# Kernel tuning notes

Hardware: AMD Instinct MI355X
Metric: run time of the kernel (lower is better)

The kernel has to match this reference:

```python
import jax, jax.numpy as jnp
import numpy as np

B, T, D, H = 2, 2048, 1024, 16
DH = D // H

def setup_inputs() -> dict:
    key = jax.random.key(0)
    ks = jax.random.split(key, 6)
    s = 0.02
    return {
        "x": jax.random.normal(ks[0], (B, T, D), jnp.float32),
        "Wq": jax.random.normal(ks[1], (D, D), jnp.float32) * s,
        "Wk": jax.random.normal(ks[2], (D, D), jnp.float32) * s,
        "Wv": jax.random.normal(ks[3], (D, D), jnp.float32) * s,
        "Wo": jax.random.normal(ks[4], (D, D), jnp.float32) * s,
        "bo": jnp.zeros((D,), jnp.float32),
    }

def reference(x, Wq, Wk, Wv, Wo, bo):
    Bx, Tx, _ = x.shape
    # project and split heads: [B, H, T, DH]
    q = (x @ Wq).reshape(Bx, Tx, H, DH).transpose(0, 2, 1, 3)
    k = (x @ Wk).reshape(Bx, Tx, H, DH).transpose(0, 2, 1, 3)
    v = (x @ Wv).reshape(Bx, Tx, H, DH).transpose(0, 2, 1, 3)
    scores = jnp.einsum("bhqd,bhkd->bhqk", q, k)  # [B,H,T,T]
    causal = jnp.triu(jnp.ones((Tx, Tx), bool), k=1)  # True above diagonal
    scores = jnp.where(causal, -jnp.inf, scores)
    # original scales AFTER masking (equivalent math)
    w = jax.nn.softmax(scores / jnp.sqrt(jnp.float32(DH)), axis=-1)
    # dropout p=0.0 -> identity
    ctx = jnp.einsum("bhqk,bhkd->bhqd", w, v)
    ctx = ctx.transpose(0, 2, 1, 3).reshape(Bx, Tx, D)
    return ctx @ Wo + bo
```

## Files before the change

kernel.cpp:

```cpp
#include <hip/hip_runtime.h>
#include <hip/hip_bf16.h>


typedef __bf16 bf16x8 __attribute__((ext_vector_type(8)));
typedef __bf16 bf16x4 __attribute__((ext_vector_type(4)));
typedef float  f32x4  __attribute__((ext_vector_type(4)));

#define Bx 2
#define Tx 2048
#define Dx 1024
#define Hx 16
#define DHx 64

__global__ __launch_bounds__(256) void prep(const float* __restrict__ x,
                                            const float* __restrict__ W0,
                                            const float* __restrict__ W1,
                                            const float* __restrict__ W2,
                                            const float* __restrict__ W3,
                                            __bf16* __restrict__ xb,
                                            __bf16* __restrict__ Wt) {
    const int z = blockIdx.z;
    if (z == 0) {
        const int blk = blockIdx.y * 16 + blockIdx.x;
        const float* xp = x + (size_t)blk * 16384;
        __bf16* xo = xb + (size_t)blk * 16384;
#pragma unroll
        for (int i = 0; i < 16; i++) {
            float4 v = *(const float4*)(xp + i * 1024 + threadIdx.x * 4);
            bf16x4 o;
            o[0] = (__bf16)v.x; o[1] = (__bf16)v.y; o[2] = (__bf16)v.z; o[3] = (__bf16)v.w;
            *(bf16x4*)(xo + i * 1024 + threadIdx.x * 4) = o;
        }
        return;
    }
    __shared__ float tile[64][65];
    const float* W = (z == 1) ? W0 : (z == 2) ? W1 : (z == 3) ? W2 : W3;
    __bf16* o = Wt + (size_t)(z - 1) * Dx * Dx;
    int k0 = blockIdx.x * 64, n0 = blockIdx.y * 64;
    int t = threadIdx.x;
    int cc = t & 63, rbase = t >> 6;
#pragma unroll
    for (int i = 0; i < 16; i++) {
        int rr = rbase + i * 4;
        tile[rr][cc] = W[(size_t)(k0 + rr) * Dx + n0 + cc];
    }
    __syncthreads();
#pragma unroll
    for (int i = 0; i < 16; i++) {
        int rr = rbase + i * 4;
        o[(size_t)(n0 + rr) * Dx + k0 + cc] = (__bf16)tile[cc][rr];
    }
}

static __device__ __forceinline__ void gload16(const __bf16* g, __bf16* l) {
    __builtin_amdgcn_global_load_lds((const __attribute__((address_space(1))) void*)g,
                                     (__attribute__((address_space(3))) void*)l, 16, 0, 0);
}

__global__ __launch_bounds__(256, 3) void gemm_qkv(const __bf16* __restrict__ A,
                                                   const __bf16* __restrict__ BT,
                                                   __bf16* __restrict__ Qb,
                                                   __bf16* __restrict__ Kb,
                                                   __bf16* __restrict__ Vt) {
    __shared__ __bf16 As[2][128 * 32];
    __shared__ __bf16 Bs[2][128 * 32];
    const int t = threadIdx.x;
    const int lane = t & 63, wave = t >> 6;
    const int lane15 = lane & 15, quad = lane >> 4;
    const int m0 = blockIdx.x * 128, n0 = blockIdx.y * 128;
    const int wm = wave & 1, wn = wave >> 1;

    const int sr = wave * 16 + (lane >> 2);
    const int sc = (lane & 3) * 8;
    const __bf16* Ag = A + (size_t)(m0 + sr) * Dx + sc;
    const __bf16* Bg = BT + (size_t)(n0 + sr) * Dx + sc;
    __bf16* As00 = &As[0][(wave * 16) * 32];
    __bf16* As01 = &As[0][(64 + wave * 16) * 32];
    __bf16* As10 = &As[1][(wave * 16) * 32];
    __bf16* As11 = &As[1][(64 + wave * 16) * 32];
    __bf16* Bs00 = &Bs[0][(wave * 16) * 32];
    __bf16* Bs01 = &Bs[0][(64 + wave * 16) * 32];
    __bf16* Bs10 = &Bs[1][(wave * 16) * 32];
    __bf16* Bs11 = &Bs[1][(64 + wave * 16) * 32];

    f32x4 acc[4][4];
#pragma unroll
    for (int i = 0; i < 4; i++)
#pragma unroll
        for (int j = 0; j < 4; j++) acc[i][j] = (f32x4){0.f, 0.f, 0.f, 0.f};

    for (int k0 = 0; k0 < Dx; k0 += 64) {
        gload16(Ag, As00);
        gload16(Ag + 64 * Dx, As01);
        gload16(Ag + 32, As10);
        gload16(Ag + 64 * Dx + 32, As11);
        gload16(Bg, Bs00);
        gload16(Bg + 64 * Dx, Bs01);
        gload16(Bg + 32, Bs10);
        gload16(Bg + 64 * Dx + 32, Bs11);
        Ag += 64; Bg += 64;
        __syncthreads();
#pragma unroll
        for (int half = 0; half < 2; half++) {
            bf16x8 af[4], bfr[4];
#pragma unroll
            for (int i = 0; i < 4; i++)
                af[i] = *(const bf16x8*)&As[half][(wm * 64 + i * 16 + lane15) * 32 + quad * 8];
#pragma unroll
            for (int j = 0; j < 4; j++)
                bfr[j] = *(const bf16x8*)&Bs[half][(wn * 64 + j * 16 + lane15) * 32 + quad * 8];
#pragma unroll
            for (int mt = 0; mt < 4; mt++)
#pragma unroll
                for (int nt = 0; nt < 4; nt++)
                    acc[mt][nt] = __builtin_amdgcn_mfma_f32_16x16x32_bf16(af[mt], bfr[nt], acc[mt][nt], 0, 0, 0);
        }
        __syncthreads();
    }

    const int z = n0 >> 10;
    if (z < 2) {
        __bf16* outp = z ? Kb : Qb;
        const float scale = z ? 1.0f : 0.18033688011112042f;
#pragma unroll
        for (int mt = 0; mt < 4; mt++)
#pragma unroll
            for (int nt = 0; nt < 4; nt++) {
                const int cc = (n0 + wn * 64 + nt * 16 + lane15) & 1023;
                const int h = cc >> 6, dh = cc & 63;
#pragma unroll
                for (int r4 = 0; r4 < 4; r4++) {
                    const int row = m0 + wm * 64 + mt * 16 + quad * 4 + r4;
                    const int b = row >> 11, tt = row & 2047;
                    outp[(((size_t)(b * Hx + h) * Tx + tt) << 6) + dh] =
                        (__bf16)(acc[mt][nt][r4] * scale);
                }
            }
    } else {
#pragma unroll
        for (int mt = 0; mt < 4; mt++)
#pragma unroll
            for (int nt = 0; nt < 4; nt++) {
                const int cc = (n0 + wn * 64 + nt * 16 + lane15) & 1023;
                const int h = cc >> 6, dh = cc & 63;
#pragma unroll
                for (int r4 = 0; r4 < 4; r4++) {
                    const int row = m0 + wm * 64 + mt * 16 + quad * 4 + r4;
                    const int b = row >> 11, tt = row & 2047;
                    Vt[((size_t)(b * Hx + h) * DHx + dh) * Tx + tt] = (__bf16)acc[mt][nt][r4];
                }
            }
    }
}

__global__ __launch_bounds__(256, 2) void gemm_out(const __bf16* __restrict__ A,
                                                   const __bf16* __restrict__ BT,
                                                   float* __restrict__ outf,
                                                   const float* __restrict__ bias) {
    __shared__ __bf16 As[2][128 * 32];
    __shared__ __bf16 Bs[2][64 * 32];
    const int t = threadIdx.x;
    const int lane = t & 63, wave = t >> 6;
    const int lane15 = lane & 15, quad = lane >> 4;
    const int m0 = blockIdx.x * 128, n0 = blockIdx.y * 64;
    const int wm = wave & 1, wn = wave >> 1;

    const int sr = wave * 16 + (lane >> 2), sc = (lane & 3) * 8;
    const __bf16* Ag = A + (size_t)(m0 + sr) * Dx + sc;
    const __bf16* Bg = BT + (size_t)(n0 + sr) * Dx + sc;
    __bf16* As00 = &As[0][(wave * 16) * 32];
    __bf16* As01 = &As[0][(64 + wave * 16) * 32];
    __bf16* As10 = &As[1][(wave * 16) * 32];
    __bf16* As11 = &As[1][(64 + wave * 16) * 32];
    __bf16* Bs0  = &Bs[0][(wave * 16) * 32];
    __bf16* Bs1  = &Bs[1][(wave * 16) * 32];

    f32x4 acc[4][2];
#pragma unroll
    for (int i = 0; i < 4; i++)
#pragma unroll
        for (int j = 0; j < 2; j++) acc[i][j] = (f32x4){0.f, 0.f, 0.f, 0.f};

    for (int k0 = 0; k0 < Dx; k0 += 64) {
        gload16(Ag, As00);
        gload16(Ag + 64 * Dx, As01);
        gload16(Ag + 32, As10);
        gload16(Ag + 64 * Dx + 32, As11);
        gload16(Bg, Bs0);
        gload16(Bg + 32, Bs1);
        Ag += 64; Bg += 64;
        __syncthreads();
#pragma unroll
        for (int half = 0; half < 2; half++) {
            bf16x8 af[4], bfr[2];
#pragma unroll
            for (int i = 0; i < 4; i++)
                af[i] = *(const bf16x8*)&As[half][(wm * 64 + i * 16 + lane15) * 32 + quad * 8];
#pragma unroll
            for (int j = 0; j < 2; j++)
                bfr[j] = *(const bf16x8*)&Bs[half][(wn * 32 + j * 16 + lane15) * 32 + quad * 8];
#pragma unroll
            for (int mt = 0; mt < 4; mt++)
#pragma unroll
                for (int nt = 0; nt < 2; nt++)
                    acc[mt][nt] = __builtin_amdgcn_mfma_f32_16x16x32_bf16(af[mt], bfr[nt], acc[mt][nt], 0, 0, 0);
        }
        __syncthreads();
    }

#pragma unroll
    for (int mt = 0; mt < 4; mt++)
#pragma unroll
        for (int nt = 0; nt < 2; nt++) {
            const int col = n0 + wn * 32 + nt * 16 + lane15;
#pragma unroll
            for (int r4 = 0; r4 < 4; r4++) {
                const int row = m0 + wm * 64 + mt * 16 + quad * 4 + r4;
                outf[(size_t)row * Dx + col] = acc[mt][nt][r4] + bias[col];
            }
        }
}

__global__ __launch_bounds__(256) void attn_mfma(const __bf16* __restrict__ Q,
                                                 const __bf16* __restrict__ K,
                                                 const __bf16* __restrict__ Vt,
                                                 __bf16* __restrict__ ctx) {
    __shared__ __bf16 Ks[2][64 * 72];
    __shared__ __bf16 Vs[2][64 * 72];
    __shared__ __bf16 Ps[64 * 72];
    const int t = threadIdx.x;
    const int lane = t & 63, wave = t >> 6;
    const int lane15 = lane & 15, quad = lane >> 4;
    const int id = blockIdx.x;
    const int bh = id & 31, p = id >> 5;
    const int b = bh >> 4, h = bh & 15;
    const size_t headoff = ((size_t)(b * Hx + h)) * Tx * DHx;
    const __bf16* Kbase = K + headoff;
    const __bf16* Vbase = Vt + headoff;
    const int sr = t >> 2, sc = (t & 3) * 16;

    for (int cidx = 0; cidx < 2; cidx++) {
        const int chunk = (cidx == 0) ? (31 - p) : p;
        const int ktiles = chunk + 1;
        const int q0 = chunk * 64;
        const int qg = q0 + wave * 16 + quad * 4;

        bf16x8 qf0, qf1;
        {
            const __bf16* Qp = Q + headoff + (size_t)(q0 + wave * 16 + lane15) * 64 + quad * 8;
            qf0 = *(const bf16x8*)Qp;
            qf1 = *(const bf16x8*)(Qp + 32);
        }
        f32x4 o[4];
#pragma unroll
        for (int i = 0; i < 4; i++) o[i] = (f32x4){0.f, 0.f, 0.f, 0.f};
        float lpart[4] = {0.f, 0.f, 0.f, 0.f};

        bf16x8 kpre0, kpre1, vpre0, vpre1;
        {
            const __bf16* Kp = Kbase + (size_t)sr * 64 + sc;
            kpre0 = *(const bf16x8*)Kp; kpre1 = *(const bf16x8*)(Kp + 8);
            const __bf16* Vp = Vbase + (size_t)sr * Tx + sc;
            vpre0 = *(const bf16x8*)Vp; vpre1 = *(const bf16x8*)(Vp + 8);
        }
        __syncthreads();
        *(bf16x8*)&Ks[0][sr * 72 + sc] = kpre0;
        *(bf16x8*)&Ks[0][sr * 72 + sc + 8] = kpre1;
        *(bf16x8*)&Vs[0][sr * 72 + sc] = vpre0;
        *(bf16x8*)&Vs[0][sr * 72 + sc + 8] = vpre1;
        __syncthreads();

        for (int kt = 0; kt < ktiles; kt++) {
            const int cur = kt & 1;
            const bool more = (kt + 1 < ktiles);
            if (more) {
                const __bf16* Kp = Kbase + (size_t)((kt + 1) * 64 + sr) * 64 + sc;
                kpre0 = *(const bf16x8*)Kp; kpre1 = *(const bf16x8*)(Kp + 8);
                const __bf16* Vp = Vbase + (size_t)sr * Tx + (kt + 1) * 64 + sc;
                vpre0 = *(const bf16x8*)Vp; vpre1 = *(const bf16x8*)(Vp + 8);
            }

            f32x4 s[4];
            __builtin_amdgcn_s_setprio(1);
#pragma unroll
            for (int nt = 0; nt < 4; nt++) {
                s[nt] = (f32x4){0.f, 0.f, 0.f, 0.f};
                bf16x8 b0 = *(const bf16x8*)&Ks[cur][(nt * 16 + lane15) * 72 + quad * 8];
                s[nt] = __builtin_amdgcn_mfma_f32_16x16x32_bf16(qf0, b0, s[nt], 0, 0, 0);
                bf16x8 b1 = *(const bf16x8*)&Ks[cur][(nt * 16 + lane15) * 72 + 32 + quad * 8];
                s[nt] = __builtin_amdgcn_mfma_f32_16x16x32_bf16(qf1, b1, s[nt], 0, 0, 0);
            }
            __builtin_amdgcn_s_setprio(0);

            if (kt == ktiles - 1) {
#pragma unroll
                for (int nt = 0; nt < 4; nt++)
#pragma unroll
                    for (int reg = 0; reg < 4; reg++) {
                        float e = __builtin_amdgcn_exp2f(s[nt][reg]);
                        if (nt * 16 + lane15 > wave * 16 + quad * 4 + reg) e = 0.f;
                        lpart[reg] += e;
                        Ps[(wave * 16 + quad * 4 + reg) * 72 + nt * 16 + lane15] = (__bf16)e;
                    }
            } else {
#pragma unroll
                for (int nt = 0; nt < 4; nt++)
#pragma unroll
                    for (int reg = 0; reg < 4; reg++) {
                        float e = __builtin_amdgcn_exp2f(s[nt][reg]);
                        lpart[reg] += e;
                        Ps[(wave * 16 + quad * 4 + reg) * 72 + nt * 16 + lane15] = (__bf16)e;
                    }
            }

            bf16x8 pa0 = *(const bf16x8*)&Ps[(wave * 16 + lane15) * 72 + quad * 8];
            bf16x8 pa1 = *(const bf16x8*)&Ps[(wave * 16 + lane15) * 72 + 32 + quad * 8];
            __builtin_amdgcn_s_setprio(1);
#pragma unroll
            for (int dt = 0; dt < 4; dt++) {
                bf16x8 vb0 = *(const bf16x8*)&Vs[cur][(dt * 16 + lane15) * 72 + quad * 8];
                o[dt] = __builtin_amdgcn_mfma_f32_16x16x32_bf16(pa0, vb0, o[dt], 0, 0, 0);
                bf16x8 vb1 = *(const bf16x8*)&Vs[cur][(dt * 16 + lane15) * 72 + 32 + quad * 8];
                o[dt] = __builtin_amdgcn_mfma_f32_16x16x32_bf16(pa1, vb1, o[dt], 0, 0, 0);
            }
            __builtin_amdgcn_s_setprio(0);

            if (more) {
                const int nxt = cur ^ 1;
                *(bf16x8*)&Ks[nxt][sr * 72 + sc] = kpre0;
                *(bf16x8*)&Ks[nxt][sr * 72 + sc + 8] = kpre1;
                *(bf16x8*)&Vs[nxt][sr * 72 + sc] = vpre0;
                *(bf16x8*)&Vs[nxt][sr * 72 + sc + 8] = vpre1;
            }
            __syncthreads();
        }

        float inv[4];
#pragma unroll
        for (int reg = 0; reg < 4; reg++) {
            float l = lpart[reg];
#pragma unroll
            for (int off = 1; off < 16; off <<= 1) l += __shfl_xor(l, off);
            inv[reg] = 1.f / l;
        }
#pragma unroll
        for (int dt = 0; dt < 4; dt++)
#pragma unroll
            for (int reg = 0; reg < 4; reg++) {
                int q = q0 + wave * 16 + quad * 4 + reg;
                ctx[(((size_t)(b * Tx + q)) * Hx + h) * 64 + dt * 16 + lane15] =
                    (__bf16)(o[dt][reg] * inv[reg]);
            }
    }
}

extern "C" void kernel_launch(void* const* d_in, const int* in_sizes, int n_in,
                              void* d_out, int out_size, void* d_ws, size_t ws_size,
                              hipStream_t stream) {
    const float* x  = (const float*)d_in[0];
    const float* Wq = (const float*)d_in[1];
    const float* Wk = (const float*)d_in[2];
    const float* Wv = (const float*)d_in[3];
    const float* Wo = (const float*)d_in[4];
    const float* bo = (const float*)d_in[5];
    float* out = (float*)d_out;

    char* ws = (char*)d_ws;
    __bf16* xb  = (__bf16*)(ws + 0);
    __bf16* Wt  = (__bf16*)(ws + (8ull << 20));
    __bf16* Qb  = (__bf16*)(ws + (16ull << 20));
    __bf16* Kb  = (__bf16*)(ws + (24ull << 20));
    __bf16* Vtg = (__bf16*)(ws + (32ull << 20));
    __bf16* ctx = (__bf16*)(ws + (40ull << 20));

    prep<<<dim3(16, 16, 5), 256, 0, stream>>>(x, Wq, Wk, Wv, Wo, xb, Wt);

    gemm_qkv<<<dim3(Bx * Tx / 128, 3 * Dx / 128), 256, 0, stream>>>(xb, Wt, Qb, Kb, Vtg);

    attn_mfma<<<dim3(512), 256, 0, stream>>>(Qb, Kb, Vtg, ctx);

    gemm_out<<<dim3(Bx * Tx / 128, Dx / 64), 256, 0, stream>>>(ctx, Wt + 3 * (1u << 20), out, bo);
}
```

Measured before the change: 172.8 us.

## Enlarge attention query tile to 128 rows with two row-tiles per wave

The attention kernel now gives each block a single 128-row query chunk instead of two paired 64-row chunks. Each wave now handles 32 query rows as two MFMA row tiles that share every K/V fragment loaded from LDS, which halves K/V staging traffic per query row. Waves whose rows lie entirely before the final diagonal key tile skip it, and heavy chunks are scheduled first to offset the lost pairing balance. The cost is more registers (launch bounds now request 2 blocks per CU), a larger P buffer in shared memory, and coarser load balance across the causal triangle.

```diff
diff --git a/kernel.cpp b/kernel.cpp
--- a/kernel.cpp
+++ b/kernel.cpp
@@ -221,137 +221,166 @@
         }
 }
 
-__global__ __launch_bounds__(256) void attn_mfma(const __bf16* __restrict__ Q,
-                                                 const __bf16* __restrict__ K,
-                                                 const __bf16* __restrict__ Vt,
-                                                 __bf16* __restrict__ ctx) {
+__global__ __launch_bounds__(256, 2) void attn_mfma(const __bf16* __restrict__ Q,
+                                                    const __bf16* __restrict__ K,
+                                                    const __bf16* __restrict__ Vt,
+                                                    __bf16* __restrict__ ctx) {
     __shared__ __bf16 Ks[2][64 * 72];
     __shared__ __bf16 Vs[2][64 * 72];
-    __shared__ __bf16 Ps[64 * 72];
+    __shared__ __bf16 Ps[128 * 72];
     const int t = threadIdx.x;
     const int lane = t & 63, wave = t >> 6;
     const int lane15 = lane & 15, quad = lane >> 4;
     const int id = blockIdx.x;
-    const int bh = id & 31, p = id >> 5;
+    const int bh = id & 31, ord = id >> 5;
+    const int chunk = (ord < 8) ? (15 - ord) : (ord - 8);
     const int b = bh >> 4, h = bh & 15;
+    const int ktiles = 2 * chunk + 2;
+    const int q0 = chunk * 128;
     const size_t headoff = ((size_t)(b * Hx + h)) * Tx * DHx;
     const __bf16* Kbase = K + headoff;
     const __bf16* Vbase = Vt + headoff;
     const int sr = t >> 2, sc = (t & 3) * 16;
-
-    for (int cidx = 0; cidx < 2; cidx++) {
-        const int chunk = (cidx == 0) ? (31 - p) : p;
-        const int ktiles = chunk + 1;
-        const int q0 = chunk * 64;
-        const int qg = q0 + wave * 16 + quad * 4;
-
-        bf16x8 qf0, qf1;
-        {
-            const __bf16* Qp = Q + headoff + (size_t)(q0 + wave * 16 + lane15) * 64 + quad * 8;
-            qf0 = *(const bf16x8*)Qp;
-            qf1 = *(const bf16x8*)(Qp + 32);
-        }
-        f32x4 o[4];
-#pragma unroll
-        for (int i = 0; i < 4; i++) o[i] = (f32x4){0.f, 0.f, 0.f, 0.f};
-        float lpart[4] = {0.f, 0.f, 0.f, 0.f};
-
-        bf16x8 kpre0, kpre1, vpre0, vpre1;
-        {
-            const __bf16* Kp = Kbase + (size_t)sr * 64 + sc;
+    const int wb = wave * 32;
+
+    bf16x8 qf00, qf01, qf10, qf11;
+    {
+        const __bf16* Qp = Q + headoff + (size_t)(q0 + wb + lane15) * 64 + quad * 8;
+        qf00 = *(const bf16x8*)Qp;
+        qf01 = *(const bf16x8*)(Qp + 32);
+        qf10 = *(const bf16x8*)(Qp + 16 * 64);
+        qf11 = *(const bf16x8*)(Qp + 16 * 64 + 32);
+    }
+    f32x4 o0[4], o1[4];
+#pragma unroll
+    for (int i = 0; i < 4; i++) {
+        o0[i] = (f32x4){0.f, 0.f, 0.f, 0.f};
+        o1[i] = (f32x4){0.f, 0.f, 0.f, 0.f};
+    }
+    float lp0[4] = {0.f, 0.f, 0.f, 0.f};
+    float lp1[4] = {0.f, 0.f, 0.f, 0.f};
+
+    bf16x8 kpre0, kpre1, vpre0, vpre1;
+    {
+        const __bf16* Kp = Kbase + (size_t)sr * 64 + sc;
+        kpre0 = *(const bf16x8*)Kp; kpre1 = *(const bf16x8*)(Kp + 8);
+        const __bf16* Vp = Vbase + (size_t)sr * Tx + sc;
+        vpre0 = *(const bf16x8*)Vp; vpre1 = *(const bf16x8*)(Vp + 8);
+    }
+    *(bf16x8*)&Ks[0][sr * 72 + sc] = kpre0;
+    *(bf16x8*)&Ks[0][sr * 72 + sc + 8] = kpre1;
+    *(bf16x8*)&Vs[0][sr * 72 + sc] = vpre0;
+    *(bf16x8*)&Vs[0][sr * 72 + sc + 8] = vpre1;
+    __syncthreads();
+
+    for (int kt = 0; kt < ktiles; kt++) {
+        const int cur = kt & 1;
+        const bool more = (kt + 1 < ktiles);
+        if (more) {
+            const __bf16* Kp = Kbase + (size_t)((kt + 1) * 64 + sr) * 64 + sc;
             kpre0 = *(const bf16x8*)Kp; kpre1 = *(const bf16x8*)(Kp + 8);
-            const __bf16* Vp = Vbase + (size_t)sr * Tx + sc;
+            const __bf16* Vp = Vbase + (size_t)sr * Tx + (kt + 1) * 64 + sc;
             vpre0 = *(const bf16x8*)Vp; vpre1 = *(const bf16x8*)(Vp + 8);
         }
-        __syncthreads();
-        *(bf16x8*)&Ks[0][sr * 72 + sc] = kpre0;
-        *(bf16x8*)&Ks[0][sr * 72 + sc + 8] = kpre1;
-        *(bf16x8*)&Vs[0][sr * 72 + sc] = vpre0;
-        *(bf16x8*)&Vs[0][sr * 72 + sc + 8] = vpre1;
-        __syncthreads();
-
-        for (int kt = 0; kt < ktiles; kt++) {
-            const int cur = kt & 1;
-            const bool more = (kt + 1 < ktiles);
-            if (more) {
-                const __bf16* Kp = Kbase + (size_t)((kt + 1) * 64 + sr) * 64 + sc;
-                kpre0 = *(const bf16x8*)Kp; kpre1 = *(const bf16x8*)(Kp + 8);
-                const __bf16* Vp = Vbase + (size_t)sr * Tx + (kt + 1) * 64 + sc;
-                vpre0 = *(const bf16x8*)Vp; vpre1 = *(const bf16x8*)(Vp + 8);
-            }
-
-            f32x4 s[4];
+
+        const bool active = !(kt == ktiles - 1 && wave < 2);
+        if (active) {
+            f32x4 s0[4], s1[4];
             __builtin_amdgcn_s_setprio(1);
 #pragma unroll
             for (int nt = 0; nt < 4; nt++) {
-                s[nt] = (f32x4){0.f, 0.f, 0.f, 0.f};
                 bf16x8 b0 = *(const bf16x8*)&Ks[cur][(nt * 16 + lane15) * 72 + quad * 8];
-                s[nt] = __builtin_amdgcn_mfma_f32_16x16x32_bf16(qf0, b0, s[nt], 0, 0, 0);
                 bf16x8 b1 = *(const bf16x8*)&Ks[cur][(nt * 16 + lane15) * 72 + 32 + quad * 8];
-                s[nt] = __builtin_amdgcn_mfma_f32_16x16x32_bf16(qf1, b1, s[nt], 0, 0, 0);
+                s0[nt] = (f32x4){0.f, 0.f, 0.f, 0.f};
+                s0[nt] = __builtin_amdgcn_mfma_f32_16x16x32_bf16(qf00, b0, s0[nt], 0, 0, 0);
+                s0[nt] = __builtin_amdgcn_mfma_f32_16x16x32_bf16(qf01, b1, s0[nt], 0, 0, 0);
+                s1[nt] = (f32x4){0.f, 0.f, 0.f, 0.f};
+                s1[nt] = __builtin_amdgcn_mfma_f32_16x16x32_bf16(qf10, b0, s1[nt], 0, 0, 0);
+                s1[nt] = __builtin_amdgcn_mfma_f32_16x16x32_bf16(qf11, b1, s1[nt], 0, 0, 0);
             }
             __builtin_amdgcn_s_setprio(0);
 
-            if (kt == ktiles - 1) {
+            if (kt >= ktiles - 2) {
+                const int koff = (kt - (ktiles - 2)) * 64;
+                const int qb = wb + quad * 4 - koff;
 #pragma unroll
                 for (int nt = 0; nt < 4; nt++)
 #pragma unroll
                     for (int reg = 0; reg < 4; reg++) {
-                        float e = __builtin_amdgcn_exp2f(s[nt][reg]);
-                        if (nt * 16 + lane15 > wave * 16 + quad * 4 + reg) e = 0.f;
-                        lpart[reg] += e;
-                        Ps[(wave * 16 + quad * 4 + reg) * 72 + nt * 16 + lane15] = (__bf16)e;
+                        const int key = nt * 16 + lane15;
+                        float e0 = __builtin_amdgcn_exp2f(s0[nt][reg]);
+                        if (key > qb + reg) e0 = 0.f;
+                        lp0[reg] += e0;
+                        Ps[(wb + quad * 4 + reg) * 72 + key] = (__bf16)e0;
+                        float e1 = __builtin_amdgcn_exp2f(s1[nt][reg]);
+                        if (key > qb + 16 + reg) e1 = 0.f;
+                        lp1[reg] += e1;
+                        Ps[(wb + 16 + quad * 4 + reg) * 72 + key] = (__bf16)e1;
                     }
             } else {
 #pragma unroll
                 for (int nt = 0; nt < 4; nt++)
 #pragma unroll
                     for (int reg = 0; reg < 4; reg++) {
-                        float e = __builtin_amdgcn_exp2f(s[nt][reg]);
-                        lpart[reg] += e;
-                        Ps[(wave * 16 + quad * 4 + reg) * 72 + nt * 16 + lane15] = (__bf16)e;
+                        const int key = nt * 16 + lane15;
+                        float e0 = __builtin_amdgcn_exp2f(s0[nt][reg]);
+                        lp0[reg] += e0;
+                        Ps[(wb + quad * 4 + reg) * 72 + key] = (__bf16)e0;
+                        float e1 = __builtin_amdgcn_exp2f(s1[nt][reg]);
+                        lp1[reg] += e1;
+                        Ps[(wb + 16 + quad * 4 + reg) * 72 + key] = (__bf16)e1;
                     }
             }
 
-            bf16x8 pa0 = *(const bf16x8*)&Ps[(wave * 16 + lane15) * 72 + quad * 8];
-            bf16x8 pa1 = *(const bf16x8*)&Ps[(wave * 16 + lane15) * 72 + 32 + quad * 8];
+            bf16x8 pa00 = *(const bf16x8*)&Ps[(wb + lane15) * 72 + quad * 8];
+            bf16x8 pa01 = *(const bf16x8*)&Ps[(wb + lane15) * 72 + 32 + quad * 8];
+            bf16x8 pa10 = *(const bf16x8*)&Ps[(wb + 16 + lane15) * 72 + quad * 8];
+            bf16x8 pa11 = *(const bf16x8*)&Ps[(wb + 16 + lane15) * 72 + 32 + quad * 8];
             __builtin_amdgcn_s_setprio(1);
 #pragma unroll
             for (int dt = 0; dt < 4; dt++) {
                 bf16x8 vb0 = *(const bf16x8*)&Vs[cur][(dt * 16 + lane15) * 72 + quad * 8];
-                o[dt] = __builtin_amdgcn_mfma_f32_16x16x32_bf16(pa0, vb0, o[dt], 0, 0, 0);
                 bf16x8 vb1 = *(const bf16x8*)&Vs[cur][(dt * 16 + lane15) * 72 + 32 + quad * 8];
-                o[dt] = __builtin_amdgcn_mfma_f32_16x16x32_bf16(pa1, vb1, o[dt], 0, 0, 0);
+                o0[dt] = __builtin_amdgcn_mfma_f32_16x16x32_bf16(pa00, vb0, o0[dt], 0, 0, 0);
+                o0[dt] = __builtin_amdgcn_mfma_f32_16x16x32_bf16(pa01, vb1, o0[dt], 0, 0, 0);
+                o1[dt] = __builtin_amdgcn_mfma_f32_16x16x32_bf16(pa10, vb0, o1[dt], 0, 0, 0);
+                o1[dt] = __builtin_amdgcn_mfma_f32_16x16x32_bf16(pa11, vb1, o1[dt], 0, 0, 0);
             }
             __builtin_amdgcn_s_setprio(0);
-
-            if (more) {
-                const int nxt = cur ^ 1;
-                *(bf16x8*)&Ks[nxt][sr * 72 + sc] = kpre0;
-                *(bf16x8*)&Ks[nxt][sr * 72 + sc + 8] = kpre1;
-                *(bf16x8*)&Vs[nxt][sr * 72 + sc] = vpre0;
-                *(bf16x8*)&Vs[nxt][sr * 72 + sc + 8] = vpre1;
-            }
-            __syncthreads();
-        }
-
-        float inv[4];
+        }
+
+        if (more) {
+            const int nxt = cur ^ 1;
+            *(bf16x8*)&Ks[nxt][sr * 72 + sc] = kpre0;
+            *(bf16x8*)&Ks[nxt][sr * 72 + sc + 8] = kpre1;
+            *(bf16x8*)&Vs[nxt][sr * 72 + sc] = vpre0;
+            *(bf16x8*)&Vs[nxt][sr * 72 + sc + 8] = vpre1;
+        }
+        __syncthreads();
+    }
+
+    float inv0[4], inv1[4];
+#pragma unroll
+    for (int reg = 0; reg < 4; reg++) {
+        float l0 = lp0[reg], l1 = lp1[reg];
+#pragma unroll
+        for (int off = 1; off < 16; off <<= 1) {
+            l0 += __shfl_xor(l0, off);
+            l1 += __shfl_xor(l1, off);
+        }
+        inv0[reg] = 1.f / l0;
+        inv1[reg] = 1.f / l1;
+    }
+#pragma unroll
+    for (int dt = 0; dt < 4; dt++)
 #pragma unroll
         for (int reg = 0; reg < 4; reg++) {
-            float l = lpart[reg];
-#pragma unroll
-            for (int off = 1; off < 16; off <<= 1) l += __shfl_xor(l, off);
-            inv[reg] = 1.f / l;
-        }
-#pragma unroll
-        for (int dt = 0; dt < 4; dt++)
-#pragma unroll
-            for (int reg = 0; reg < 4; reg++) {
-                int q = q0 + wave * 16 + quad * 4 + reg;
-                ctx[(((size_t)(b * Tx + q)) * Hx + h) * 64 + dt * 16 + lane15] =
-                    (__bf16)(o[dt][reg] * inv[reg]);
-            }
-    }
+            const int q = q0 + wb + quad * 4 + reg;
+            ctx[(((size_t)(b * Tx + q)) * Hx + h) * 64 + dt * 16 + lane15] =
+                (__bf16)(o0[dt][reg] * inv0[reg]);
+            ctx[(((size_t)(b * Tx + q + 16)) * Hx + h) * 64 + dt * 16 + lane15] =
+                (__bf16)(o1[dt][reg] * inv1[reg]);
+        }
 }
 
 extern "C" void kernel_launch(void* const* d_in, const int* in_sizes, int n_in,
```

Result: slower. 181.7 us (+5.1%).
